# Kernel optimization log

Hardware: AMD Instinct MI355X
Metric: run time of the kernel (lower is better)

## Reference

```python
import jax, jax.numpy as jnp
import numpy as np

N_ELEC = 8192   # electrons (nodes)
N_NUC = 512     # nuclei
EMB = 256       # embedding_dim
KER = 256       # kernel_dim
DF = 64         # dist_feat_dim
MID = 128       # round(sqrt(DF*KER)), log-interpolated hidden width of w-MLP
E = 131072      # edges per edge type


def _ssp(x):
    # shifted softplus, deepqmc default activation: log(0.5*exp(x) + 0.5)
    return jax.nn.softplus(x) - jnp.log(2.0)


def setup_inputs() -> dict:
    key = jax.random.key(0)
    ks = jax.random.split(key, 24)
    def nrm(k, shape, scale):
        return jax.random.normal(k, shape, dtype=jnp.float32) * scale
    inp = {}
    inp['electrons'] = nrm(ks[0], (N_ELEC, EMB), 1.0)
    inp['nuclei'] = nrm(ks[1], (N_NUC, KER), 1.0)
    for i, lbl in enumerate(['same', 'anti', 'n']):
        inp[f'dist_{lbl}'] = jax.random.uniform(ks[2 + i], (E, DF), dtype=jnp.float32)
        inp[f'w1_{lbl}'] = nrm(ks[5 + i], (DF, MID), DF ** -0.5)
        inp[f'b1_{lbl}'] = jnp.zeros((MID,), jnp.float32)
        inp[f'w2_{lbl}'] = nrm(ks[8 + i], (MID, KER), MID ** -0.5)
        inp[f'g_{lbl}'] = nrm(ks[11 + i], (KER, EMB), KER ** -0.5)
    inp['h_w'] = nrm(ks[14], (EMB, KER), EMB ** -0.5)
    inp['senders_same'] = jax.random.randint(ks[15], (E,), 0, N_ELEC)
    inp['senders_anti'] = jax.random.randint(ks[16], (E,), 0, N_ELEC)
    inp['senders_n'] = jax.random.randint(ks[17], (E,), 0, N_NUC)
    inp['receivers_same'] = jax.random.randint(ks[18], (E,), 0, N_ELEC)
    inp['receivers_anti'] = jax.random.randint(ks[19], (E,), 0, N_ELEC)
    inp['receivers_n'] = jax.random.randint(ks[20], (E,), 0, N_ELEC)
    return inp


def reference(electrons, nuclei, dist_same, dist_anti, dist_n,
              w1_same, b1_same, w2_same, w1_anti, b1_anti, w2_anti,
              w1_n, b1_n, w2_n, g_same, g_anti, g_n, h_w,
              senders_same, senders_anti, senders_n,
              receivers_same, receivers_anti, receivers_n):
    def w_mlp(d, w1, b1, w2):
        # MLP with ('log', 2) hidden layers: linear+bias -> SSP -> last linear (no bias)
        return _ssp(d @ w1 + b1) @ w2

    # per-edge filters from distance features: [E, KER]
    we_same = w_mlp(dist_same, w1_same, b1_same, w2_same)
    we_anti = w_mlp(dist_anti, w1_anti, b1_anti, w2_anti)
    we_n = w_mlp(dist_n, w1_n, b1_n, w2_n)

    # shared h (single bias-free linear) on gathered sender electrons: [E, KER]
    hx_same = electrons[senders_same] @ h_w
    hx_anti = electrons[senders_anti] @ h_w

    weh_same = we_same * hx_same
    weh_anti = we_anti * hx_anti
    weh_n = we_n * nuclei[senders_n]

    # scatter-sum messages to receiver electrons: [N_ELEC, KER]
    z_same = jax.ops.segment_sum(weh_same, receivers_same, num_segments=N_ELEC)
    z_anti = jax.ops.segment_sum(weh_anti, receivers_anti, num_segments=N_ELEC)
    z_n = jax.ops.segment_sum(weh_n, receivers_n, num_segments=N_ELEC)

    # per-label g (single bias-free linear) + residual update, order matches original
    return electrons + (z_n @ g_n + z_same @ g_same + z_anti @ g_anti)
```

## Files before the change

kernel.cpp:

```cpp
#include <hip/hip_runtime.h>
#include <stdint.h>


#define N_ELEC 8192
#define N_NUC  512
#define EMB    256
#define KER    256
#define DF     64
#define MID    128
#define NEDGE  131072
#define RPS    8256
#define CSTR   272

using u16 = unsigned short;
using u64 = unsigned long long;
typedef short short8 __attribute__((ext_vector_type(8)));
typedef float f32x4 __attribute__((ext_vector_type(4)));

__device__ __forceinline__ float bf2f(u16 h) {
  return __uint_as_float(((unsigned)h) << 16);
}
__device__ __forceinline__ u16 f2bf(float f) {
  unsigned u = __float_as_uint(f);
  return (u16)((u + 0x7FFFu + ((u >> 16) & 1u)) >> 16);
}
__device__ __forceinline__ unsigned pkbf(float a, float b) {
  return ((unsigned)f2bf(b) << 16) | (unsigned)f2bf(a);
}
__device__ __forceinline__ float ssp_fast(float x) {
  const float e = __expf(-fabsf(x));
  return fmaxf(x, 0.f) + __logf(fmaf(0.5f, e, 0.5f));
}

__device__ __forceinline__ void bar_lds() {
  __builtin_amdgcn_sched_barrier(0);
  asm volatile("s_waitcnt lgkmcnt(0)" ::: "memory");
  __builtin_amdgcn_s_barrier();
  __builtin_amdgcn_sched_barrier(0);
}

__device__ __forceinline__ void stage_f32x32(const float* g0, int stride_e,
                                             int kt, char* lds, int tid) {
#pragma unroll
  for (int k = 0; k < 2; ++k) {
    const int idx2 = k * 256 + tid;
    const int row = idx2 >> 4, cp = idx2 & 15;
    const float2 v = *(const float2*)(g0 + (long)row * stride_e + kt + cp * 2);
    *(unsigned*)(lds + row * 64 + cp * 4) = pkbf(v.x, v.y);
  }
}

__global__ __launch_bounds__(256) void k_setup(
    const float* h_w, const float* w1s, const float* w1a, const float* w1n,
    const float* w2s, const float* w2a, const float* w2n, const float* gs,
    const float* ga, const float* gn, u16* hwT, u16* w1T, u16* w2T, u16* gT,
    float4* z, int* cnt) {
  const int b = blockIdx.x;
  if (b < 6144) {
    z[b * 256 + threadIdx.x] = (float4){0.f, 0.f, 0.f, 0.f};
    return;
  }
  if (b < 6240) {
    cnt[(b - 6144) * 256 + threadIdx.x] = 0;
    return;
  }
  int i = (b - 6240) * 256 + threadIdx.x;
  if (i < 65536) {
    int n = i >> 8, k = i & 255;
    hwT[i] = f2bf(h_w[k * 256 + n]);
    return;
  }
  int j = i - 65536;
  if (j < 24576) {
    int t = j >> 13, jj = j & 8191, n = jj >> 6, k = jj & 63;
    const float* w1 = t == 0 ? w1s : (t == 1 ? w1a : w1n);
    w1T[j] = f2bf(w1[k * 128 + n]);
    return;
  }
  j -= 24576;
  if (j < 98304) {
    int t = j >> 15, jj = j & 32767, n = jj >> 7, k = jj & 127;
    const float* w2 = t == 0 ? w2s : (t == 1 ? w2a : w2n);
    w2T[j] = f2bf(w2[k * 256 + n]);
    return;
  }
  j -= 98304;
  if (j < 196608) {
    int n = j / 768, q = j % 768, t = q >> 8, k = q & 255;
    const float* g = t == 0 ? gs : (t == 1 ? ga : gn);
    gT[j] = f2bf(g[k * 256 + n]);
  }
}

__global__ __launch_bounds__(256) void k_hist(const int* r0, const int* r1,
                                              const int* r2, int* cnt) {
  const int t = blockIdx.z;
  const int* rcv = t == 0 ? r0 : (t == 1 ? r1 : r2);
  const int e = blockIdx.x * 256 + threadIdx.x;
  atomicAdd(&cnt[t * N_ELEC + rcv[e]], 1);
}

__global__ __launch_bounds__(256) void k_scan(const int* cnt, int* rowptr,
                                              int* cursor) {
  const int t = blockIdx.x, tid = threadIdx.x;
  __shared__ int part[256];
  const int* c = cnt + t * N_ELEC;
  int s = 0;
#pragma unroll
  for (int i = 0; i < 32; ++i) s += c[tid * 32 + i];
  part[tid] = s;
  __syncthreads();
  for (int off = 1; off < 256; off <<= 1) {
    int v = (tid >= off) ? part[tid - off] : 0;
    __syncthreads();
    part[tid] += v;
    __syncthreads();
  }
  int run = (tid == 0) ? 0 : part[tid - 1];
  int* rp = rowptr + t * RPS;
  int* cu = cursor + t * N_ELEC;
  for (int i = 0; i < 32; ++i) {
    rp[tid * 32 + i] = run;
    cu[tid * 32 + i] = run;
    run += c[tid * 32 + i];
  }
  if (tid == 255) rp[N_ELEC] = run;
}

__global__ __launch_bounds__(256) void k_place(const int* r0, const int* r1,
                                               const int* r2, const int* s0,
                                               const int* s1, const int* s2,
                                               int* cursor, u64* pk) {
  const int t = blockIdx.z;
  const int* rcv = t == 0 ? r0 : (t == 1 ? r1 : r2);
  const int* snd = t == 0 ? s0 : (t == 1 ? s1 : s2);
  const int e = blockIdx.x * 256 + threadIdx.x;
  const int rr = rcv[e];
  const int pos = atomicAdd(&cursor[t * N_ELEC + rr], 1);
  pk[t * NEDGE + pos] =
      (u64)(unsigned)e | ((u64)(unsigned)snd[e] << 17) | ((u64)(unsigned)rr << 30);
}

__global__ __launch_bounds__(256) void k_he(const float* elec, const u16* hwT,
                                            u16* he) {
  __shared__ __align__(16) char As[2048];
  const int tid = threadIdx.x;
  const int m0 = blockIdx.x * 32;
  const int l = tid & 63, lane15 = l & 15, quad = l >> 4, wv = tid >> 6;
  const int nw = wv * 64;
  f32x4 acc[2][4];
#pragma unroll
  for (int i = 0; i < 2; ++i)
#pragma unroll
    for (int j = 0; j < 4; ++j) acc[i][j] = (f32x4){0.f, 0.f, 0.f, 0.f};
  for (int kt = 0; kt < 256; kt += 32) {
    stage_f32x32(elec + (long)m0 * 256, 256, kt, As, tid);
    __syncthreads();
    short8 af[2], bf[4];
#pragma unroll
    for (int i = 0; i < 2; ++i)
      af[i] = *(const short8*)(As + (i * 16 + lane15) * 64 + quad * 16);
#pragma unroll
    for (int i = 0; i < 4; ++i)
      bf[i] = *(const short8*)(hwT + (nw + i * 16 + lane15) * 256 + kt +
                               quad * 8);
#pragma unroll
    for (int mi = 0; mi < 2; ++mi)
#pragma unroll
      for (int ni = 0; ni < 4; ++ni)
        acc[mi][ni] = __builtin_amdgcn_mfma_f32_16x16x32_bf16(
            af[mi], bf[ni], acc[mi][ni], 0, 0, 0);
    __syncthreads();
  }
#pragma unroll
  for (int mi = 0; mi < 2; ++mi)
#pragma unroll
    for (int r = 0; r < 4; ++r) {
      const int row = m0 + mi * 16 + quad * 4 + r;
#pragma unroll
      for (int ni = 0; ni < 4; ++ni) {
        const int col = nw + ni * 16 + lane15;
        he[row * 256 + col] = f2bf(acc[mi][ni][r]);
      }
    }
}

__global__ __launch_bounds__(256, 3) void k_edge(
    const float* d0, const float* d1, const float* d2, const float* b0,
    const float* b1p, const float* b2, const u16* w1T, const u16* w2T,
    const u16* he, const float* nucf, const u64* pk, float* z) {
  __shared__ char mid[128 * CSTR];
  __shared__ char hc[64 * CSTR];
  __shared__ int snd_l[128], rcv_l[128];

  const int t = blockIdx.z;
  const int m0 = blockIdx.x * 128;
  const int tid = threadIdx.x;
  const float* dist = t == 0 ? d0 : (t == 1 ? d1 : d2);
  const float* bias = t == 0 ? b0 : (t == 1 ? b1p : b2);
  const u16* w1t = w1T + t * 8192;
  const u16* w2t = w2T + t * 32768;
  const bool is_nuc = (t == 2);
  const u64* pkt = pk + (size_t)t * NEDGE + m0;

  if (tid < 128) {
    const u64 rec = pkt[tid];
    snd_l[tid] = (int)((rec >> 17) & 0x1FFFu);
    rcv_l[tid] = (int)(rec >> 30);
  }

  int rows[4];
#pragma unroll
  for (int s = 0; s < 4; ++s)
    rows[s] = (int)(pkt[(s * 256 + tid) >> 3] & 0x1FFFFu);
#pragma unroll
  for (int j = 0; j < 2; ++j)
#pragma unroll
    for (int s = 0; s < 4; ++s) {
      const int idx = s * 256 + tid, row = idx >> 3, ch = idx & 7;
      const float4 v =
          *(const float4*)(dist + (long)rows[s] * 64 + j * 32 + ch * 4);
      uint2 p;
      p.x = pkbf(v.x, v.y);
      p.y = pkbf(v.z, v.w);
      *(uint2*)(mid + j * 8192 + row * 64 + ch * 8) = p;
    }
  bar_lds();

  const int l = tid & 63, lane15 = l & 15, quad = l >> 4, wv = tid >> 6;
  const int mw = (wv >> 1) * 64, nw = (wv & 1) * 64;

  f32x4 acc[4][4];
#pragma unroll
  for (int i = 0; i < 4; ++i)
#pragma unroll
    for (int j = 0; j < 4; ++j) acc[i][j] = (f32x4){0.f, 0.f, 0.f, 0.f};
#pragma unroll
  for (int j = 0; j < 2; ++j) {
    short8 af[4], bf[4];
#pragma unroll
    for (int i = 0; i < 4; ++i) {
      af[i] = *(const short8*)(mid + j * 8192 + (mw + i * 16 + lane15) * 64 +
                               quad * 16);
      bf[i] = *(const short8*)(w1t + (nw + i * 16 + lane15) * 64 + j * 32 +
                               quad * 8);
    }
#pragma unroll
    for (int mi = 0; mi < 4; ++mi)
#pragma unroll
      for (int ni = 0; ni < 4; ++ni)
        acc[mi][ni] = __builtin_amdgcn_mfma_f32_16x16x32_bf16(
            af[mi], bf[ni], acc[mi][ni], 0, 0, 0);
  }
  bar_lds();

#pragma unroll
  for (int mi = 0; mi < 4; ++mi)
#pragma unroll
    for (int r = 0; r < 4; ++r) {
      const int row = mw + mi * 16 + quad * 4 + r;
#pragma unroll
      for (int ni = 0; ni < 4; ++ni) {
        const int col = nw + ni * 16 + lane15;
        const float x = acc[mi][ni][r] + bias[col];
        *(u16*)(mid + row * CSTR + col * 2) = f2bf(ssp_fast(x));
      }
    }
  bar_lds();

  for (int n0 = 0; n0 < 256; n0 += 128) {
#pragma unroll
    for (int i = 0; i < 4; ++i)
#pragma unroll
      for (int j = 0; j < 4; ++j) acc[i][j] = (f32x4){0.f, 0.f, 0.f, 0.f};
#pragma unroll
    for (int kt = 0; kt < 128; kt += 32) {
      short8 af[4], bf[4];
#pragma unroll
      for (int i = 0; i < 4; ++i) {
        af[i] = *(const short8*)(mid + (mw + i * 16 + lane15) * CSTR + kt * 2 +
                                 quad * 16);
        bf[i] = *(const short8*)(w2t + (n0 + nw + i * 16 + lane15) * 128 + kt +
                                 quad * 8);
      }
#pragma unroll
      for (int mi = 0; mi < 4; ++mi)
#pragma unroll
        for (int ni = 0; ni < 4; ++ni)
          acc[mi][ni] = __builtin_amdgcn_mfma_f32_16x16x32_bf16(
              af[mi], bf[ni], acc[mi][ni], 0, 0, 0);
    }

    for (int h = 0; h < 2; ++h) {
      const int rbase = h * 64;
      if (!is_nuc) {
#pragma unroll
        for (int c = 0; c < 4; ++c) {
          const int chunk = c * 256 + tid;
          const int row = chunk >> 4, off = chunk & 15;
          const uint4 v =
              *(const uint4*)((const char*)he +
                              (size_t)snd_l[rbase + row] * 512 + n0 * 2 +
                              off * 16);
          *(uint4*)(hc + row * CSTR + off * 16) = v;
        }
      } else {
#pragma unroll
        for (int c = 0; c < 4; ++c) {
          const int chunk = c * 256 + tid;
          const int row = chunk >> 4, off = chunk & 15;
          const char* src = (const char*)nucf +
                            (size_t)snd_l[rbase + row] * 1024 + n0 * 4 +
                            off * 32;
          const float4 a = *(const float4*)src;
          const float4 b = *(const float4*)(src + 16);
          uint4 p;
          p.x = pkbf(a.x, a.y);
          p.y = pkbf(a.z, a.w);
          p.z = pkbf(b.x, b.y);
          p.w = pkbf(b.z, b.w);
          *(uint4*)(hc + row * CSTR + off * 16) = p;
        }
      }
      bar_lds();

      if ((wv >> 1) == h) {
#pragma unroll
        for (int mi = 0; mi < 4; ++mi)
#pragma unroll
          for (int r = 0; r < 4; ++r) {
            const int lrow = mi * 16 + quad * 4 + r;
#pragma unroll
            for (int ni = 0; ni < 4; ++ni) {
              const int col = nw + ni * 16 + lane15;
              u16* p = (u16*)(hc + lrow * CSTR) + col;
              *p = f2bf(acc[mi][ni][r] * bf2f(*p));
            }
          }
      }
      bar_lds();

      {
        const int cp = l;
        const int rbeg = wv * 16, rend = rbeg + 16;
        float a0 = 0.f, a1 = 0.f;
        int cur = rcv_l[rbase + rbeg];
        for (int row = rbeg; row < rend; ++row) {
          const unsigned p = *(const unsigned*)(hc + row * CSTR + cp * 4);
          a0 += __uint_as_float(p << 16);
          a1 += __uint_as_float(p & 0xffff0000u);
          const int nxt = (row + 1 < rend) ? rcv_l[rbase + row + 1] : -1;
          if (nxt != cur) {
            float* zp = z + (size_t)cur * 768 + t * 256 + n0 + cp * 2;
            unsafeAtomicAdd(zp, a0);
            unsafeAtomicAdd(zp + 1, a1);
            a0 = a1 = 0.f;
            cur = nxt;
          }
        }
      }
      bar_lds();
    }
  }
}

__global__ __launch_bounds__(256) void k_final(const float* z, const u16* gT,
                                               const float* elec, float* out) {
  __shared__ __align__(16) char As[2048];
  const int tid = threadIdx.x;
  const int m0 = blockIdx.x * 32;
  const int l = tid & 63, lane15 = l & 15, quad = l >> 4, wv = tid >> 6;
  const int nw = wv * 64;
  f32x4 acc[2][4];
#pragma unroll
  for (int i = 0; i < 2; ++i)
#pragma unroll
    for (int j = 0; j < 4; ++j) acc[i][j] = (f32x4){0.f, 0.f, 0.f, 0.f};
  for (int kt = 0; kt < 768; kt += 32) {
    stage_f32x32(z + (long)m0 * 768, 768, kt, As, tid);
    __syncthreads();
    short8 af[2], bf[4];
#pragma unroll
    for (int i = 0; i < 2; ++i)
      af[i] = *(const short8*)(As + (i * 16 + lane15) * 64 + quad * 16);
#pragma unroll
    for (int i = 0; i < 4; ++i)
      bf[i] = *(const short8*)(gT + (nw + i * 16 + lane15) * 768 + kt +
                               quad * 8);
#pragma unroll
    for (int mi = 0; mi < 2; ++mi)
#pragma unroll
      for (int ni = 0; ni < 4; ++ni)
        acc[mi][ni] = __builtin_amdgcn_mfma_f32_16x16x32_bf16(
            af[mi], bf[ni], acc[mi][ni], 0, 0, 0);
    __syncthreads();
  }
#pragma unroll
  for (int mi = 0; mi < 2; ++mi)
#pragma unroll
    for (int r = 0; r < 4; ++r) {
      const int row = m0 + mi * 16 + quad * 4 + r;
#pragma unroll
      for (int ni = 0; ni < 4; ++ni) {
        const int col = nw + ni * 16 + lane15;
        out[row * 256 + col] = acc[mi][ni][r] + elec[row * 256 + col];
      }
    }
}

extern "C" void kernel_launch(void* const* d_in, const int* in_sizes, int n_in,
                              void* d_out, int out_size, void* d_ws,
                              size_t ws_size, hipStream_t stream) {
  int I_dist[3], I_w1[3], I_b1[3], I_w2[3], I_g[3], I_hw;
  if (in_sizes[3] == 64 * 128) {
    for (int t = 0; t < 3; ++t) {
      I_dist[t] = 2 + t * 5 + 0;
      I_w1[t] = 2 + t * 5 + 1;
      I_b1[t] = 2 + t * 5 + 2;
      I_w2[t] = 2 + t * 5 + 3;
      I_g[t] = 2 + t * 5 + 4;
    }
    I_hw = 17;
  } else {
    I_dist[0] = 2; I_dist[1] = 3; I_dist[2] = 4;
    I_w1[0] = 5;  I_b1[0] = 6;  I_w2[0] = 7;
    I_w1[1] = 8;  I_b1[1] = 9;  I_w2[1] = 10;
    I_w1[2] = 11; I_b1[2] = 12; I_w2[2] = 13;
    I_g[0] = 14; I_g[1] = 15; I_g[2] = 16;
    I_hw = 17;
  }
  const int I_snd[3] = {18, 19, 20};
  const int I_rcv[3] = {21, 22, 23};

  char* ws = (char*)d_ws;
  u16* he = (u16*)(ws + 0);
  u16* hwT = (u16*)(ws + 4194304);
  u16* w1T = (u16*)(ws + 4325376);
  u16* w2T = (u16*)(ws + 4374528);
  u16* gT = (u16*)(ws + 4571136);
  float* z = (float*)(ws + 4964352);
  int* cnt = (int*)(ws + 30130176);
  int* rowptr = (int*)(ws + 30228480);
  int* cursor = (int*)(ws + 30327552);
  u64* pk = (u64*)(ws + 30425856);

  const float* elec = (const float*)d_in[0];
  const float* nuc = (const float*)d_in[1];
  const int* s0 = (const int*)d_in[I_snd[0]];
  const int* s1 = (const int*)d_in[I_snd[1]];
  const int* s2 = (const int*)d_in[I_snd[2]];
  const int* r0 = (const int*)d_in[I_rcv[0]];
  const int* r1 = (const int*)d_in[I_rcv[1]];
  const int* r2 = (const int*)d_in[I_rcv[2]];

  k_setup<<<7744, 256, 0, stream>>>(
      (const float*)d_in[I_hw], (const float*)d_in[I_w1[0]],
      (const float*)d_in[I_w1[1]], (const float*)d_in[I_w1[2]],
      (const float*)d_in[I_w2[0]], (const float*)d_in[I_w2[1]],
      (const float*)d_in[I_w2[2]], (const float*)d_in[I_g[0]],
      (const float*)d_in[I_g[1]], (const float*)d_in[I_g[2]], hwT, w1T, w2T,
      gT, (float4*)z, cnt);

  k_hist<<<dim3(NEDGE / 256, 1, 3), 256, 0, stream>>>(r0, r1, r2, cnt);
  k_scan<<<3, 256, 0, stream>>>(cnt, rowptr, cursor);
  k_place<<<dim3(NEDGE / 256, 1, 3), 256, 0, stream>>>(r0, r1, r2, s0, s1, s2,
                                                       cursor, pk);

  k_he<<<N_ELEC / 32, 256, 0, stream>>>(elec, hwT, he);

  k_edge<<<dim3(NEDGE / 128, 1, 3), 256, 0, stream>>>(
      (const float*)d_in[I_dist[0]], (const float*)d_in[I_dist[1]],
      (const float*)d_in[I_dist[2]], (const float*)d_in[I_b1[0]],
      (const float*)d_in[I_b1[1]], (const float*)d_in[I_b1[2]], w1T, w2T, he,
      nuc, pk, z);

  k_final<<<N_ELEC / 32, 256, 0, stream>>>(z, gT, elec, (float*)d_out);
}
```

Before: 401.0 us.

## Merge histogram into setup, fuse placement with he GEMM, stage full A tiles

The histogram atomics move into the setup kernel, and the count buffer is cleared by a memset issued beforehand. Edge placement and the he GEMM are merged into one launch, with block ranges picking the task. Both the he and final GEMMs now stage the whole 32-row A tile into padded LDS once instead of reloading per k-step, which removes the per-iteration barriers. This cuts the number of kernel launches and the sync overhead, at the cost of more LDS per block, which may lower occupancy.

```diff
diff --git a/kernel.cpp b/kernel.cpp
--- a/kernel.cpp
+++ b/kernel.cpp
@@ -11,6 +11,8 @@
 #define NEDGE  131072
 #define RPS    8256
 #define CSTR   272
+#define ASTR_HE 528
+#define ASTR_FN 1552
 
 using u16 = unsigned short;
 using u64 = unsigned long long;
@@ -39,32 +41,26 @@
   __builtin_amdgcn_sched_barrier(0);
 }
 
-__device__ __forceinline__ void stage_f32x32(const float* g0, int stride_e,
-                                             int kt, char* lds, int tid) {
-#pragma unroll
-  for (int k = 0; k < 2; ++k) {
-    const int idx2 = k * 256 + tid;
-    const int row = idx2 >> 4, cp = idx2 & 15;
-    const float2 v = *(const float2*)(g0 + (long)row * stride_e + kt + cp * 2);
-    *(unsigned*)(lds + row * 64 + cp * 4) = pkbf(v.x, v.y);
-  }
-}
-
 __global__ __launch_bounds__(256) void k_setup(
     const float* h_w, const float* w1s, const float* w1a, const float* w1n,
     const float* w2s, const float* w2a, const float* w2n, const float* gs,
-    const float* ga, const float* gn, u16* hwT, u16* w1T, u16* w2T, u16* gT,
-    float4* z, int* cnt) {
+    const float* ga, const float* gn, const int* r0, const int* r1,
+    const int* r2, u16* hwT, u16* w1T, u16* w2T, u16* gT, float4* z,
+    int* cnt) {
   const int b = blockIdx.x;
   if (b < 6144) {
     z[b * 256 + threadIdx.x] = (float4){0.f, 0.f, 0.f, 0.f};
     return;
   }
-  if (b < 6240) {
-    cnt[(b - 6144) * 256 + threadIdx.x] = 0;
-    return;
-  }
-  int i = (b - 6240) * 256 + threadIdx.x;
+  if (b >= 7648) {
+    const int eb = b - 7648;
+    const int t = eb >> 9;
+    const int* rcv = t == 0 ? r0 : (t == 1 ? r1 : r2);
+    const int e = ((eb & 511) << 8) + threadIdx.x;
+    atomicAdd(&cnt[t * N_ELEC + rcv[e]], 1);
+    return;
+  }
+  int i = (b - 6144) * 256 + threadIdx.x;
   if (i < 65536) {
     int n = i >> 8, k = i & 255;
     hwT[i] = f2bf(h_w[k * 256 + n]);
@@ -90,14 +86,6 @@
     const float* g = t == 0 ? gs : (t == 1 ? ga : gn);
     gT[j] = f2bf(g[k * 256 + n]);
   }
-}
-
-__global__ __launch_bounds__(256) void k_hist(const int* r0, const int* r1,
-                                              const int* r2, int* cnt) {
-  const int t = blockIdx.z;
-  const int* rcv = t == 0 ? r0 : (t == 1 ? r1 : r2);
-  const int e = blockIdx.x * 256 + threadIdx.x;
-  atomicAdd(&cnt[t * N_ELEC + rcv[e]], 1);
 }
 
 __global__ __launch_bounds__(256) void k_scan(const int* cnt, int* rowptr,
@@ -127,25 +115,32 @@
   if (tid == 255) rp[N_ELEC] = run;
 }
 
-__global__ __launch_bounds__(256) void k_place(const int* r0, const int* r1,
-                                               const int* r2, const int* s0,
-                                               const int* s1, const int* s2,
-                                               int* cursor, u64* pk) {
-  const int t = blockIdx.z;
-  const int* rcv = t == 0 ? r0 : (t == 1 ? r1 : r2);
-  const int* snd = t == 0 ? s0 : (t == 1 ? s1 : s2);
-  const int e = blockIdx.x * 256 + threadIdx.x;
-  const int rr = rcv[e];
-  const int pos = atomicAdd(&cursor[t * N_ELEC + rr], 1);
-  pk[t * NEDGE + pos] =
-      (u64)(unsigned)e | ((u64)(unsigned)snd[e] << 17) | ((u64)(unsigned)rr << 30);
-}
-
-__global__ __launch_bounds__(256) void k_he(const float* elec, const u16* hwT,
-                                            u16* he) {
-  __shared__ __align__(16) char As[2048];
-  const int tid = threadIdx.x;
-  const int m0 = blockIdx.x * 32;
+__global__ __launch_bounds__(256) void k_place_he(
+    const int* r0, const int* r1, const int* r2, const int* s0, const int* s1,
+    const int* s2, int* cursor, u64* pk, const float* elec, const u16* hwT,
+    u16* he) {
+  __shared__ __align__(16) char As[32 * ASTR_HE];
+  const int bid = blockIdx.x, tid = threadIdx.x;
+  if (bid < 1536) {
+    const int t = bid >> 9;
+    const int* rcv = t == 0 ? r0 : (t == 1 ? r1 : r2);
+    const int* snd = t == 0 ? s0 : (t == 1 ? s1 : s2);
+    const int e = ((bid & 511) << 8) + tid;
+    const int rr = rcv[e];
+    const int pos = atomicAdd(&cursor[t * N_ELEC + rr], 1);
+    pk[t * NEDGE + pos] = (u64)(unsigned)e | ((u64)(unsigned)snd[e] << 17) |
+                          ((u64)(unsigned)rr << 30);
+    return;
+  }
+  const int m0 = (bid - 1536) * 32;
+#pragma unroll
+  for (int i = 0; i < 16; ++i) {
+    const int idx = i * 256 + tid;
+    const int row = idx >> 7, cp = idx & 127;
+    const float2 v = *(const float2*)(elec + (long)(m0 + row) * 256 + cp * 2);
+    *(unsigned*)(As + row * ASTR_HE + cp * 4) = pkbf(v.x, v.y);
+  }
+  __syncthreads();
   const int l = tid & 63, lane15 = l & 15, quad = l >> 4, wv = tid >> 6;
   const int nw = wv * 64;
   f32x4 acc[2][4];
@@ -154,12 +149,11 @@
 #pragma unroll
     for (int j = 0; j < 4; ++j) acc[i][j] = (f32x4){0.f, 0.f, 0.f, 0.f};
   for (int kt = 0; kt < 256; kt += 32) {
-    stage_f32x32(elec + (long)m0 * 256, 256, kt, As, tid);
-    __syncthreads();
     short8 af[2], bf[4];
 #pragma unroll
     for (int i = 0; i < 2; ++i)
-      af[i] = *(const short8*)(As + (i * 16 + lane15) * 64 + quad * 16);
+      af[i] = *(const short8*)(As + (i * 16 + lane15) * ASTR_HE + kt * 2 +
+                               quad * 16);
 #pragma unroll
     for (int i = 0; i < 4; ++i)
       bf[i] = *(const short8*)(hwT + (nw + i * 16 + lane15) * 256 + kt +
@@ -170,7 +164,6 @@
       for (int ni = 0; ni < 4; ++ni)
         acc[mi][ni] = __builtin_amdgcn_mfma_f32_16x16x32_bf16(
             af[mi], bf[ni], acc[mi][ni], 0, 0, 0);
-    __syncthreads();
   }
 #pragma unroll
   for (int mi = 0; mi < 2; ++mi)
@@ -366,9 +359,20 @@
 
 __global__ __launch_bounds__(256) void k_final(const float* z, const u16* gT,
                                                const float* elec, float* out) {
-  __shared__ __align__(16) char As[2048];
+  __shared__ __align__(16) char As[32 * ASTR_FN];
   const int tid = threadIdx.x;
   const int m0 = blockIdx.x * 32;
+#pragma unroll
+  for (int i = 0; i < 24; ++i) {
+    const int idx = i * 256 + tid;
+    const int row = idx / 192, q = idx % 192;
+    const float4 v = *(const float4*)(z + (long)(m0 + row) * 768 + q * 4);
+    uint2 p;
+    p.x = pkbf(v.x, v.y);
+    p.y = pkbf(v.z, v.w);
+    *(uint2*)(As + row * ASTR_FN + q * 8) = p;
+  }
+  __syncthreads();
   const int l = tid & 63, lane15 = l & 15, quad = l >> 4, wv = tid >> 6;
   const int nw = wv * 64;
   f32x4 acc[2][4];
@@ -377,12 +381,11 @@
 #pragma unroll
     for (int j = 0; j < 4; ++j) acc[i][j] = (f32x4){0.f, 0.f, 0.f, 0.f};
   for (int kt = 0; kt < 768; kt += 32) {
-    stage_f32x32(z + (long)m0 * 768, 768, kt, As, tid);
-    __syncthreads();
     short8 af[2], bf[4];
 #pragma unroll
     for (int i = 0; i < 2; ++i)
-      af[i] = *(const short8*)(As + (i * 16 + lane15) * 64 + quad * 16);
+      af[i] = *(const short8*)(As + (i * 16 + lane15) * ASTR_FN + kt * 2 +
+                               quad * 16);
 #pragma unroll
     for (int i = 0; i < 4; ++i)
       bf[i] = *(const short8*)(gT + (nw + i * 16 + lane15) * 768 + kt +
@@ -393,7 +396,6 @@
       for (int ni = 0; ni < 4; ++ni)
         acc[mi][ni] = __builtin_amdgcn_mfma_f32_16x16x32_bf16(
             af[mi], bf[ni], acc[mi][ni], 0, 0, 0);
-    __syncthreads();
   }
 #pragma unroll
   for (int mi = 0; mi < 2; ++mi)
@@ -453,20 +455,20 @@
   const int* r1 = (const int*)d_in[I_rcv[1]];
   const int* r2 = (const int*)d_in[I_rcv[2]];
 
-  k_setup<<<7744, 256, 0, stream>>>(
+  hipMemsetAsync(cnt, 0, 98304, stream);
+
+  k_setup<<<9184, 256, 0, stream>>>(
       (const float*)d_in[I_hw], (const float*)d_in[I_w1[0]],
       (const float*)d_in[I_w1[1]], (const float*)d_in[I_w1[2]],
       (const float*)d_in[I_w2[0]], (const float*)d_in[I_w2[1]],
       (const float*)d_in[I_w2[2]], (const float*)d_in[I_g[0]],
-      (const float*)d_in[I_g[1]], (const float*)d_in[I_g[2]], hwT, w1T, w2T,
-      gT, (float4*)z, cnt);
-
-  k_hist<<<dim3(NEDGE / 256, 1, 3), 256, 0, stream>>>(r0, r1, r2, cnt);
+      (const float*)d_in[I_g[1]], (const float*)d_in[I_g[2]], r0, r1, r2,
+      hwT, w1T, w2T, gT, (float4*)z, cnt);
+
   k_scan<<<3, 256, 0, stream>>>(cnt, rowptr, cursor);
-  k_place<<<dim3(NEDGE / 256, 1, 3), 256, 0, stream>>>(r0, r1, r2, s0, s1, s2,
-                                                       cursor, pk);
-
-  k_he<<<N_ELEC / 32, 256, 0, stream>>>(elec, hwT, he);
+
+  k_place_he<<<1792, 256, 0, stream>>>(r0, r1, r2, s0, s1, s2, cursor, pk,
+                                       elec, hwT, he);
 
   k_edge<<<dim3(NEDGE / 128, 1, 3), 256, 0, stream>>>(
       (const float*)d_in[I_dist[0]], (const float*)d_in[I_dist[1]],
```

Result: faster. 392.0 us (-2.2%).
